# Performance work log

Hardware: AMD Instinct MI355X
Metric: run time of the kernel (lower is better)

## Reference

```python
import jax, jax.numpy as jnp
import numpy as np

H = 16  # num_attention_heads


def setup_inputs() -> dict:
    key = jax.random.key(0)
    k1, k2, k3 = jax.random.split(key, 3)
    B, S, E = 2, 2048, 1024
    return {
        "hidden_states": jax.random.normal(k1, (B, S, E), dtype=jnp.float32),
        "W_attn": jax.random.normal(k2, (E, 3 * E), dtype=jnp.float32) * 0.02,
        "b_attn": jnp.zeros((3 * E,), dtype=jnp.float32),
        "W_proj": jax.random.normal(k3, (E, E), dtype=jnp.float32) * 0.02,
        "b_proj": jnp.zeros((E,), dtype=jnp.float32),
    }


def reference(hidden_states, W_attn, b_attn, W_proj, b_proj):
    B, S, E = hidden_states.shape
    hd = E // H
    # Conv1D: x @ W + b -> [B, S, 3E]
    qkv = hidden_states @ W_attn + b_attn
    # Faithful to module: _split_heads with 3*head_dim FIRST, then split q/k/v.
    # i.e. per-head slice of size 3*hd is [q_h | k_h | v_h] (interleaved layout).
    qkv = qkv.reshape(B, S, H, 3 * hd).transpose(0, 2, 1, 3)  # [B, H, S, 3*hd]
    q, k, v = jnp.split(qkv, 3, axis=-1)                      # each [B, H, S, hd]
    # scores, scaled by sqrt(head_dim) (value.size(-1) ** 0.5)
    scores = jnp.einsum("bhqd,bhkd->bhqk", q, k) / jnp.asarray(hd, q.dtype) ** 0.5
    # causal mask via where with masked_bias = -10000.0 (not -inf), as in module
    causal = jnp.tril(jnp.ones((S, S), dtype=bool))
    scores = jnp.where(causal, scores, jnp.asarray(-10000.0, scores.dtype))
    attn_weights = jax.nn.softmax(scores, axis=-1)  # dropout p=0 -> identity
    attn_out = jnp.einsum("bhqk,bhkd->bhqd", attn_weights, v)
    attn_out = attn_out.transpose(0, 2, 1, 3).reshape(B, S, E)  # merge heads
    return attn_out @ W_proj + b_proj
```

## Files before the change

### kernel.cpp

```cpp
#include <hip/hip_runtime.h>
#include <hip/hip_bf16.h>


typedef __attribute__((ext_vector_type(4))) float f32x4;
typedef __attribute__((ext_vector_type(8))) short short8;
typedef __attribute__((ext_vector_type(2))) unsigned int uint2v;

#define AS1 __attribute__((address_space(1)))
#define AS3 __attribute__((address_space(3)))

__device__ __forceinline__ void load_lds16(const void* g, void* l) {
    __builtin_amdgcn_global_load_lds((const AS1 void*)g, (AS3 void*)l, 16, 0, 0);
}

__device__ __forceinline__ unsigned short f2bf(float f) {
    union { float f; unsigned int u; } v; v.f = f;
    unsigned int r = v.u + 0x7FFFu + ((v.u >> 16) & 1u);
    return (unsigned short)(r >> 16);
}

__device__ __forceinline__ int cvt_pk_bf16(float lo, float hi) {
    int r;
    asm("v_cvt_pk_bf16_f32 %0, %1, %2" : "=v"(r) : "v"(lo), "v"(hi));
    return r;
}

__device__ __forceinline__ void transpose_tile(
    const float* __restrict__ W, unsigned short* __restrict__ Wt,
    int K, int N, int bx, int by, int t) {
    __shared__ float tile[32][33];
    int k0 = by * 32, n0 = bx * 32;
    int r = t >> 3, c = (t & 7) * 4;
    float4 v = *(const float4*)&W[(size_t)(k0 + r) * N + n0 + c];
    tile[r][c] = v.x; tile[r][c + 1] = v.y; tile[r][c + 2] = v.z; tile[r][c + 3] = v.w;
    __syncthreads();
    int n = t >> 3; int kk = (t & 7) * 4;
    ushort4 o;
    o.x = f2bf(tile[kk + 0][n]);
    o.y = f2bf(tile[kk + 1][n]);
    o.z = f2bf(tile[kk + 2][n]);
    o.w = f2bf(tile[kk + 3][n]);
    *(ushort4*)&Wt[(size_t)(n0 + n) * K + k0 + kk] = o;
}

__global__ __launch_bounds__(256) void prep(
    const float* __restrict__ hs, unsigned short* __restrict__ Xb,
    const float* __restrict__ W_attn, unsigned short* __restrict__ WaT,
    const float* __restrict__ W_proj, unsigned short* __restrict__ WpT) {
    int bid = blockIdx.x, t = threadIdx.x;
    if (bid < 4096) {
        int i = (bid * 256 + t) * 4;
        float4 v = *(const float4*)(hs + i);
        ushort4 o;
        o.x = f2bf(v.x); o.y = f2bf(v.y); o.z = f2bf(v.z); o.w = f2bf(v.w);
        *(ushort4*)(Xb + i) = o;
    } else if (bid < 7168) {
        int r = bid - 4096;
        transpose_tile(W_attn, WaT, 1024, 3072, r % 96, r / 96, t);
    } else {
        int r = bid - 7168;
        transpose_tile(W_proj, WpT, 1024, 1024, r % 32, r / 32, t);
    }
}

__global__ __launch_bounds__(256) void gemm_qkv(
    const unsigned short* __restrict__ A,
    const unsigned short* __restrict__ Bt,
    const float* __restrict__ bias,
    unsigned short* __restrict__ qk, unsigned short* __restrict__ Vt,
    int M, int N, int K) {
    __shared__ unsigned short Sh[2][8192];
    unsigned short* Tb = &Sh[0][0];
    const int t = threadIdx.x, wave = t >> 6, lane = t & 63;
    const int l15 = lane & 15, quad = lane >> 4;
    const int m0 = blockIdx.y * 128, n0 = blockIdx.x * 128;
    const int srow = wave * 32 + (lane >> 2);
    const int sch = (lane & 3) * 8;
    const unsigned short* Ag = A + (size_t)(m0 + srow) * K + sch;
    const unsigned short* Bg = Bt + (size_t)(n0 + srow) * K + sch;
    const int wOff = wave * 1024;
    const int wm = (wave >> 1) * 64, wn = (wave & 1) * 64;
    f32x4 acc[4][4] = {};
    const int NSTEP = K / 32;
    load_lds16(Ag, &Sh[0][wOff]);
    load_lds16(Ag + (size_t)16 * K, &Sh[0][wOff + 512]);
    load_lds16(Bg, &Sh[0][4096 + wOff]);
    load_lds16(Bg + (size_t)16 * K, &Sh[0][4096 + wOff + 512]);
    for (int kt = 0; kt < NSTEP; ++kt) {
        const int cur = kt & 1;
        const unsigned short* As = &Sh[cur][0];
        const unsigned short* Bs = &Sh[cur][4096];
        __syncthreads();
        if (kt + 1 < NSTEP) {
            const int k1 = (kt + 1) * 32;
            unsigned short* An = &Sh[cur ^ 1][0];
            unsigned short* Bn = &Sh[cur ^ 1][4096];
            load_lds16(Ag + k1, An + wOff);
            load_lds16(Ag + k1 + (size_t)16 * K, An + wOff + 512);
            load_lds16(Bg + k1, Bn + wOff);
            load_lds16(Bg + k1 + (size_t)16 * K, Bn + wOff + 512);
        }
        short8 af[4], bf[4];
#pragma unroll
        for (int i = 0; i < 4; ++i) {
            af[i] = *(const short8*)&As[(wm + i * 16 + l15) * 32 + quad * 8];
            bf[i] = *(const short8*)&Bs[(wn + i * 16 + l15) * 32 + quad * 8];
        }
        __builtin_amdgcn_s_setprio(1);
#pragma unroll
        for (int mt = 0; mt < 4; ++mt)
#pragma unroll
            for (int nt = 0; nt < 4; ++nt)
                acc[mt][nt] = __builtin_amdgcn_mfma_f32_16x16x32_bf16(af[mt], bf[nt], acc[mt][nt], 0, 0, 0);
        __builtin_amdgcn_s_setprio(0);
    }
    __syncthreads();
    const int rem = n0 % 192;
#pragma unroll
    for (int mt = 0; mt < 4; ++mt) {
        int mrow = m0 + wm + mt * 16 + quad * 4;
#pragma unroll
        for (int nt = 0; nt < 4; ++nt) {
            int col = n0 + wn + nt * 16 + l15;
            float bv = bias[col];
            int h = col / 192;
            int j = col - h * 192;
            if (j < 128) {
                float sc = (j < 64) ? 0.125f : 1.0f;
#pragma unroll
                for (int r = 0; r < 4; ++r)
                    qk[(size_t)(mrow + r) * 2048 + h * 128 + j] = f2bf((acc[mt][nt][r] + bv) * sc);
            } else {
                int d = j - 128;
                int s_local = wm + mt * 16 + quad * 4;
                ushort4 pk;
                pk.x = f2bf(acc[mt][nt][0] + bv);
                pk.y = f2bf(acc[mt][nt][1] + bv);
                pk.z = f2bf(acc[mt][nt][2] + bv);
                pk.w = f2bf(acc[mt][nt][3] + bv);
                *(ushort4*)&Tb[d * 136 + s_local] = pk;
            }
        }
    }
    if (rem != 0) {
        __syncthreads();
        int vhalf = (rem == 64) ? 1 : 0;
        int h = (n0 + vhalf * 64) / 192;
        int b = m0 >> 11;
        unsigned short* vbase = Vt + ((size_t)(b * 16 + h) * 64) * 2048 + (m0 & 2047);
        int drow = t >> 4, ch = (t & 15) * 8;
#pragma unroll
        for (int rr = 0; rr < 4; ++rr) {
            int d = rr * 16 + drow;
            *(uint4*)(vbase + (size_t)d * 2048 + ch) = *(const uint4*)&Tb[d * 136 + ch];
        }
    }
}

__global__ __launch_bounds__(256) void gemm_proj(
    const unsigned short* __restrict__ A,
    const unsigned short* __restrict__ Bt,
    const float* __restrict__ bias,
    float* __restrict__ C, int M, int N, int K) {
    __shared__ unsigned short Sh[2][6144];
    const int t = threadIdx.x, wave = t >> 6, lane = t & 63;
    const int l15 = lane & 15, quad = lane >> 4;
    const int m0 = blockIdx.y * 128, n0 = blockIdx.x * 64;
    const int srowA = wave * 32 + (lane >> 2);
    const int sch = (lane & 3) * 8;
    const unsigned short* Ag = A + (size_t)(m0 + srowA) * K + sch;
    const unsigned short* Bg = Bt + (size_t)(n0 + wave * 16 + (lane >> 2)) * K + sch;
    const int aOff = wave * 1024, bOff = wave * 512;
    const int wm = (wave >> 1) * 64, wn = (wave & 1) * 32;
    f32x4 acc[4][2] = {};
    const int NSTEP = K / 32;
    load_lds16(Ag, &Sh[0][aOff]);
    load_lds16(Ag + (size_t)16 * K, &Sh[0][aOff + 512]);
    load_lds16(Bg, &Sh[0][4096 + bOff]);
    for (int kt = 0; kt < NSTEP; ++kt) {
        const int cur = kt & 1;
        const unsigned short* As = &Sh[cur][0];
        const unsigned short* Bs = &Sh[cur][4096];
        __syncthreads();
        if (kt + 1 < NSTEP) {
            const int k1 = (kt + 1) * 32;
            load_lds16(Ag + k1, &Sh[cur ^ 1][aOff]);
            load_lds16(Ag + k1 + (size_t)16 * K, &Sh[cur ^ 1][aOff + 512]);
            load_lds16(Bg + k1, &Sh[cur ^ 1][4096 + bOff]);
        }
        short8 af[4], bf[2];
#pragma unroll
        for (int i = 0; i < 4; ++i)
            af[i] = *(const short8*)&As[(wm + i * 16 + l15) * 32 + quad * 8];
#pragma unroll
        for (int i = 0; i < 2; ++i)
            bf[i] = *(const short8*)&Bs[(wn + i * 16 + l15) * 32 + quad * 8];
        __builtin_amdgcn_s_setprio(1);
#pragma unroll
        for (int mt = 0; mt < 4; ++mt)
#pragma unroll
            for (int nt = 0; nt < 2; ++nt)
                acc[mt][nt] = __builtin_amdgcn_mfma_f32_16x16x32_bf16(af[mt], bf[nt], acc[mt][nt], 0, 0, 0);
        __builtin_amdgcn_s_setprio(0);
    }
#pragma unroll
    for (int mt = 0; mt < 4; ++mt) {
        int mrow = m0 + wm + mt * 16 + quad * 4;
#pragma unroll
        for (int nt = 0; nt < 2; ++nt) {
            int col = n0 + wn + nt * 16 + l15;
            float bv = bias[col];
#pragma unroll
            for (int r = 0; r < 4; ++r)
                C[(size_t)(mrow + r) * N + col] = acc[mt][nt][r] + bv;
        }
    }
}

__device__ __forceinline__ void build_af(const int (&pk)[4][2], int qpar, short8 (&af)[2]) {
#pragma unroll
    for (int km = 0; km < 2; ++km) {
        uint2v r0 = __builtin_amdgcn_permlane32_swap(
            (unsigned)pk[2 * km][0], (unsigned)pk[2 * km + 1][0], false, false);
        uint2v r1 = __builtin_amdgcn_permlane32_swap(
            (unsigned)pk[2 * km][1], (unsigned)pk[2 * km + 1][1], false, false);
        int Ap0 = (int)r0[0], Bp0 = (int)r0[1];
        int Ap1 = (int)r1[0], Bp1 = (int)r1[1];
        int z0 = qpar ? Ap0 : Bp0;
        int z1 = qpar ? Ap1 : Bp1;
        int w0 = __builtin_amdgcn_ds_swizzle(z0, 0x401F);
        int w1 = __builtin_amdgcn_ds_swizzle(z1, 0x401F);
        int f0 = qpar ? w0 : Ap0, f1 = qpar ? w1 : Ap1;
        int g0 = qpar ? Bp0 : w0, g1 = qpar ? Bp1 : w1;
        int4 v = {f0, f1, g0, g1};
        af[km] = __builtin_bit_cast(short8, v);
    }
}

__global__ __launch_bounds__(512, 4) void attn3(
    const unsigned short* __restrict__ qk,
    const unsigned short* __restrict__ Vt,
    unsigned short* __restrict__ out) {
    const int S = 2048;
    __shared__ unsigned short Ks[2][64][72];
    __shared__ unsigned short Vts[2][64][72];
    const int t = threadIdx.x, wave = t >> 6, lane = t & 63;
    const int l15 = lane & 15, quad = lane >> 4, qpar = quad & 1;
    const int bid = blockIdx.x;
    const int qt = (bid < 256) ? (15 - (bid >> 5)) : ((bid - 256) >> 5);
    const int bh = bid & 31;
    const int b = bh >> 4, h = bh & 15;
    const unsigned short* qkb = qk + (size_t)b * S * 2048 + h * 128;
    const unsigned short* vtb = Vt + (size_t)bh * 64 * 2048;

    const int q0 = qt * 128 + wave * 16;
    short8 qf[2];
#pragma unroll
    for (int km = 0; km < 2; ++km)
        qf[km] = *(const short8*)(qkb + (size_t)(q0 + l15) * 2048 + km * 32 + quad * 8);
    f32x4 o[4] = {};
    float lrun = 0.f;

    const int srow8 = t >> 3, chunk8 = (t & 7) * 8;
    const int KT = qt * 2 + 2;

    uint4 kreg = *(const uint4*)(qkb + (size_t)srow8 * 2048 + 64 + chunk8);
    uint4 vreg = *(const uint4*)(vtb + (size_t)srow8 * 2048 + chunk8);

    const int qg = q0 + l15;
    const int qmax = q0 + 15;

    for (int kt = 0; kt < KT; ++kt) {
        const int cur = kt & 1;
        *(uint4*)&Ks[cur][srow8][chunk8] = kreg;
        *(uint4*)&Vts[cur][srow8][chunk8] = vreg;
        __syncthreads();
        if (kt + 1 < KT) {
            int kn = (kt + 1) * 64;
            kreg = *(const uint4*)(qkb + (size_t)(kn + srow8) * 2048 + 64 + chunk8);
            vreg = *(const uint4*)(vtb + (size_t)srow8 * 2048 + kn + chunk8);
        }
        const int kb = kt * 64;
        if (kb > qmax) continue;

        f32x4 s[4] = {};
        __builtin_amdgcn_s_setprio(1);
#pragma unroll
        for (int km = 0; km < 2; ++km)
#pragma unroll
            for (int nt = 0; nt < 4; ++nt) {
                short8 kf = *(const short8*)&Ks[cur][nt * 16 + l15][km * 32 + quad * 8];
                s[nt] = __builtin_amdgcn_mfma_f32_16x16x32_bf16(kf, qf[km], s[nt], 0, 0, 0);
            }
        __builtin_amdgcn_s_setprio(0);

        if (kb + 63 > q0) {
            const int ka = kb + quad * 4;
#pragma unroll
            for (int nt = 0; nt < 4; ++nt)
#pragma unroll
                for (int r = 0; r < 4; ++r)
                    if (ka + nt * 16 + r > qg) s[nt][r] = -1e30f;
        }

        int pk[4][2];
        float a0 = 0.f;
#pragma unroll
        for (int nt = 0; nt < 4; ++nt) {
            float pa[4];
#pragma unroll
            for (int r = 0; r < 4; ++r) {
                pa[r] = __expf(s[nt][r]);
                a0 += pa[r];
            }
            pk[nt][0] = cvt_pk_bf16(pa[0], pa[1]);
            pk[nt][1] = cvt_pk_bf16(pa[2], pa[3]);
        }
        lrun += a0;

        short8 af[2];
        build_af(pk, qpar, af);

        __builtin_amdgcn_s_setprio(1);
#pragma unroll
        for (int km = 0; km < 2; ++km)
#pragma unroll
            for (int nt = 0; nt < 4; ++nt) {
                short8 vf = *(const short8*)&Vts[cur][nt * 16 + l15][km * 32 + quad * 8];
                o[nt] = __builtin_amdgcn_mfma_f32_16x16x32_bf16(af[km], vf, o[nt], 0, 0, 0);
            }
        __builtin_amdgcn_s_setprio(0);
    }

    float t0 = lrun + __shfl_xor(lrun, 16);
    t0 += __shfl_xor(t0, 32);
    unsigned short* ob = out + (size_t)b * S * 1024 + h * 64;
#pragma unroll
    for (int r = 0; r < 4; ++r) {
        float i0 = 1.0f / __shfl(t0, quad * 4 + r);
        size_t r0 = (size_t)(q0 + quad * 4 + r) * 1024;
#pragma unroll
        for (int nt = 0; nt < 4; ++nt)
            ob[r0 + nt * 16 + l15] = f2bf(o[nt][r] * i0);
    }
}

extern "C" void kernel_launch(void* const* d_in, const int* in_sizes, int n_in,
                              void* d_out, int out_size, void* d_ws, size_t ws_size,
                              hipStream_t stream) {
    const float* hs     = (const float*)d_in[0];
    const float* W_attn = (const float*)d_in[1];
    const float* b_attn = (const float*)d_in[2];
    const float* W_proj = (const float*)d_in[3];
    const float* b_proj = (const float*)d_in[4];
    float* out = (float*)d_out;

    const int B = 2, S = 2048, E = 1024;
    const int M = B * S;
    const int N3 = 3 * E;

    unsigned short* Xb  = (unsigned short*)d_ws;
    unsigned short* WaT = Xb + (size_t)M * E;
    unsigned short* WpT = WaT + (size_t)N3 * E;
    unsigned short* qkb = WpT + (size_t)E * E;
    unsigned short* Vt  = qkb + (size_t)M * 2048;
    unsigned short* ao  = Vt + (size_t)M * E;

    prep<<<dim3(8192), 256, 0, stream>>>(hs, Xb, W_attn, WaT, W_proj, WpT);

    gemm_qkv<<<dim3(N3 / 128, M / 128), 256, 0, stream>>>(Xb, WaT, b_attn, qkb, Vt, M, N3, E);

    attn3<<<dim3(512), 512, 0, stream>>>(qkb, Vt, ao);

    gemm_proj<<<dim3(E / 64, M / 128), 256, 0, stream>>>(ao, WpT, b_proj, out, M, E, E);
}
```

Baseline: 176.1 us.

## Rewrite attention kernel with 32x32x16 MFMA tiles and swizzled LDS

```diff
diff --git a/kernel.cpp b/kernel.cpp
--- a/kernel.cpp
+++ b/kernel.cpp
@@ -3,6 +3,7 @@
 
 
 typedef __attribute__((ext_vector_type(4))) float f32x4;
+typedef __attribute__((ext_vector_type(16))) float f32x16;
 typedef __attribute__((ext_vector_type(8))) short short8;
 typedef __attribute__((ext_vector_type(2))) unsigned int uint2v;
 
@@ -217,35 +218,15 @@
     }
 }
 
-__device__ __forceinline__ void build_af(const int (&pk)[4][2], int qpar, short8 (&af)[2]) {
-#pragma unroll
-    for (int km = 0; km < 2; ++km) {
-        uint2v r0 = __builtin_amdgcn_permlane32_swap(
-            (unsigned)pk[2 * km][0], (unsigned)pk[2 * km + 1][0], false, false);
-        uint2v r1 = __builtin_amdgcn_permlane32_swap(
-            (unsigned)pk[2 * km][1], (unsigned)pk[2 * km + 1][1], false, false);
-        int Ap0 = (int)r0[0], Bp0 = (int)r0[1];
-        int Ap1 = (int)r1[0], Bp1 = (int)r1[1];
-        int z0 = qpar ? Ap0 : Bp0;
-        int z1 = qpar ? Ap1 : Bp1;
-        int w0 = __builtin_amdgcn_ds_swizzle(z0, 0x401F);
-        int w1 = __builtin_amdgcn_ds_swizzle(z1, 0x401F);
-        int f0 = qpar ? w0 : Ap0, f1 = qpar ? w1 : Ap1;
-        int g0 = qpar ? Bp0 : w0, g1 = qpar ? Bp1 : w1;
-        int4 v = {f0, f1, g0, g1};
-        af[km] = __builtin_bit_cast(short8, v);
-    }
-}
-
-__global__ __launch_bounds__(512, 4) void attn3(
+__global__ __launch_bounds__(256) void attn4(
     const unsigned short* __restrict__ qk,
     const unsigned short* __restrict__ Vt,
     unsigned short* __restrict__ out) {
     const int S = 2048;
-    __shared__ unsigned short Ks[2][64][72];
-    __shared__ unsigned short Vts[2][64][72];
+    __shared__ unsigned short Ks[2][4096];
+    __shared__ unsigned short Vts[2][4096];
     const int t = threadIdx.x, wave = t >> 6, lane = t & 63;
-    const int l15 = lane & 15, quad = lane >> 4, qpar = quad & 1;
+    const int l31 = lane & 31, half = lane >> 5;
     const int bid = blockIdx.x;
     const int qt = (bid < 256) ? (15 - (bid >> 5)) : ((bid - 256) >> 5);
     const int bh = bid & 31;
@@ -253,95 +234,120 @@
     const unsigned short* qkb = qk + (size_t)b * S * 2048 + h * 128;
     const unsigned short* vtb = Vt + (size_t)bh * 64 * 2048;
 
-    const int q0 = qt * 128 + wave * 16;
-    short8 qf[2];
-#pragma unroll
-    for (int km = 0; km < 2; ++km)
-        qf[km] = *(const short8*)(qkb + (size_t)(q0 + l15) * 2048 + km * 32 + quad * 8);
-    f32x4 o[4] = {};
+    const int q0 = qt * 128 + wave * 32;
+    short8 qf[4];
+#pragma unroll
+    for (int km = 0; km < 4; ++km)
+        qf[km] = *(const short8*)(qkb + (size_t)(q0 + l31) * 2048 + km * 16 + half * 8);
+
+    f32x16 o[2] = {};
     float lrun = 0.f;
 
-    const int srow8 = t >> 3, chunk8 = (t & 7) * 8;
+    const int srow = t >> 2;
+    const int c16a = (t & 3) * 2, c16b = c16a + 1;
+    const int swzA = srow * 64 + ((c16a ^ (srow & 7)) * 8);
+    const int swzB = srow * 64 + ((c16b ^ (srow & 7)) * 8);
     const int KT = qt * 2 + 2;
 
-    uint4 kreg = *(const uint4*)(qkb + (size_t)srow8 * 2048 + 64 + chunk8);
-    uint4 vreg = *(const uint4*)(vtb + (size_t)srow8 * 2048 + chunk8);
-
-    const int qg = q0 + l15;
-    const int qmax = q0 + 15;
+    uint4 kr0 = *(const uint4*)(qkb + (size_t)srow * 2048 + 64 + c16a * 8);
+    uint4 kr1 = *(const uint4*)(qkb + (size_t)srow * 2048 + 64 + c16b * 8);
+    uint4 vr0 = *(const uint4*)(vtb + (size_t)srow * 2048 + c16a * 8);
+    uint4 vr1 = *(const uint4*)(vtb + (size_t)srow * 2048 + c16b * 8);
+
+    const int qmax = q0 + 31;
+    const int ksw = l31 & 7;
+    int chs[4];
+#pragma unroll
+    for (int km = 0; km < 4; ++km)
+        chs[km] = ((km * 2 + half) ^ ksw) * 8;
+    const int krow = l31 * 64;
 
     for (int kt = 0; kt < KT; ++kt) {
         const int cur = kt & 1;
-        *(uint4*)&Ks[cur][srow8][chunk8] = kreg;
-        *(uint4*)&Vts[cur][srow8][chunk8] = vreg;
+        *(uint4*)&Ks[cur][swzA] = kr0;
+        *(uint4*)&Ks[cur][swzB] = kr1;
+        *(uint4*)&Vts[cur][swzA] = vr0;
+        *(uint4*)&Vts[cur][swzB] = vr1;
         __syncthreads();
         if (kt + 1 < KT) {
-            int kn = (kt + 1) * 64;
-            kreg = *(const uint4*)(qkb + (size_t)(kn + srow8) * 2048 + 64 + chunk8);
-            vreg = *(const uint4*)(vtb + (size_t)srow8 * 2048 + kn + chunk8);
+            const int kn = (kt + 1) * 64;
+            kr0 = *(const uint4*)(qkb + (size_t)(kn + srow) * 2048 + 64 + c16a * 8);
+            kr1 = *(const uint4*)(qkb + (size_t)(kn + srow) * 2048 + 64 + c16b * 8);
+            vr0 = *(const uint4*)(vtb + (size_t)srow * 2048 + kn + c16a * 8);
+            vr1 = *(const uint4*)(vtb + (size_t)srow * 2048 + kn + c16b * 8);
         }
         const int kb = kt * 64;
         if (kb > qmax) continue;
 
-        f32x4 s[4] = {};
+        f32x16 s[2] = {};
         __builtin_amdgcn_s_setprio(1);
 #pragma unroll
-        for (int km = 0; km < 2; ++km)
-#pragma unroll
-            for (int nt = 0; nt < 4; ++nt) {
-                short8 kf = *(const short8*)&Ks[cur][nt * 16 + l15][km * 32 + quad * 8];
-                s[nt] = __builtin_amdgcn_mfma_f32_16x16x32_bf16(kf, qf[km], s[nt], 0, 0, 0);
+        for (int nt = 0; nt < 2; ++nt)
+#pragma unroll
+            for (int km = 0; km < 4; ++km) {
+                short8 kf = *(const short8*)&Ks[cur][nt * 2048 + krow + chs[km]];
+                s[nt] = __builtin_amdgcn_mfma_f32_32x32x16_bf16(kf, qf[km], s[nt], 0, 0, 0);
             }
         __builtin_amdgcn_s_setprio(0);
 
         if (kb + 63 > q0) {
-            const int ka = kb + quad * 4;
-#pragma unroll
-            for (int nt = 0; nt < 4; ++nt)
-#pragma unroll
-                for (int r = 0; r < 4; ++r)
-                    if (ka + nt * 16 + r > qg) s[nt][r] = -1e30f;
-        }
-
-        int pk[4][2];
+#pragma unroll
+            for (int nt = 0; nt < 2; ++nt)
+#pragma unroll
+                for (int r = 0; r < 16; ++r) {
+                    int kg = kb + nt * 32 + (r & 3) + 8 * (r >> 2) + 4 * half;
+                    if (kg > q0 + l31) s[nt][r] = -1e30f;
+                }
+        }
+
+        int gd[2][4][2];
         float a0 = 0.f;
 #pragma unroll
-        for (int nt = 0; nt < 4; ++nt) {
-            float pa[4];
-#pragma unroll
-            for (int r = 0; r < 4; ++r) {
-                pa[r] = __expf(s[nt][r]);
-                a0 += pa[r];
+        for (int nt = 0; nt < 2; ++nt)
+#pragma unroll
+            for (int g = 0; g < 4; ++g) {
+                float e0 = __expf(s[nt][4 * g + 0]);
+                float e1 = __expf(s[nt][4 * g + 1]);
+                float e2 = __expf(s[nt][4 * g + 2]);
+                float e3 = __expf(s[nt][4 * g + 3]);
+                a0 += (e0 + e1) + (e2 + e3);
+                gd[nt][g][0] = cvt_pk_bf16(e0, e1);
+                gd[nt][g][1] = cvt_pk_bf16(e2, e3);
             }
-            pk[nt][0] = cvt_pk_bf16(pa[0], pa[1]);
-            pk[nt][1] = cvt_pk_bf16(pa[2], pa[3]);
-        }
         lrun += a0;
 
-        short8 af[2];
-        build_af(pk, qpar, af);
+        short8 paf[4];
+#pragma unroll
+        for (int km = 0; km < 4; ++km) {
+            const int nt = km >> 1, m = km & 1;
+            uint2v w0 = __builtin_amdgcn_permlane32_swap(
+                (unsigned)gd[nt][2 * m][0], (unsigned)gd[nt][2 * m + 1][0], false, false);
+            uint2v w1 = __builtin_amdgcn_permlane32_swap(
+                (unsigned)gd[nt][2 * m][1], (unsigned)gd[nt][2 * m + 1][1], false, false);
+            int4 v = {(int)w0[0], (int)w1[0], (int)w0[1], (int)w1[1]};
+            paf[km] = __builtin_bit_cast(short8, v);
+        }
 
         __builtin_amdgcn_s_setprio(1);
 #pragma unroll
-        for (int km = 0; km < 2; ++km)
-#pragma unroll
-            for (int nt = 0; nt < 4; ++nt) {
-                short8 vf = *(const short8*)&Vts[cur][nt * 16 + l15][km * 32 + quad * 8];
-                o[nt] = __builtin_amdgcn_mfma_f32_16x16x32_bf16(af[km], vf, o[nt], 0, 0, 0);
+        for (int nt2 = 0; nt2 < 2; ++nt2)
+#pragma unroll
+            for (int km = 0; km < 4; ++km) {
+                short8 vf = *(const short8*)&Vts[cur][nt2 * 2048 + krow + chs[km]];
+                o[nt2] = __builtin_amdgcn_mfma_f32_32x32x16_bf16(paf[km], vf, o[nt2], 0, 0, 0);
             }
         __builtin_amdgcn_s_setprio(0);
     }
 
-    float t0 = lrun + __shfl_xor(lrun, 16);
-    t0 += __shfl_xor(t0, 32);
+    float tot = lrun + __shfl_xor(lrun, 32);
     unsigned short* ob = out + (size_t)b * S * 1024 + h * 64;
 #pragma unroll
-    for (int r = 0; r < 4; ++r) {
-        float i0 = 1.0f / __shfl(t0, quad * 4 + r);
-        size_t r0 = (size_t)(q0 + quad * 4 + r) * 1024;
-#pragma unroll
-        for (int nt = 0; nt < 4; ++nt)
-            ob[r0 + nt * 16 + l15] = f2bf(o[nt][r] * i0);
+    for (int r = 0; r < 16; ++r) {
+        int ql = (r & 3) + 8 * (r >> 2) + 4 * half;
+        float inv = 1.0f / __shfl(tot, ql);
+        size_t row = (size_t)(q0 + ql) * 1024;
+        ob[row + l31] = f2bf(o[0][r] * inv);
+        ob[row + 32 + l31] = f2bf(o[1][r] * inv);
     }
 }
 
@@ -370,7 +376,7 @@
 
     gemm_qkv<<<dim3(N3 / 128, M / 128), 256, 0, stream>>>(Xb, WaT, b_attn, qkb, Vt, M, N3, E);
 
-    attn3<<<dim3(512), 512, 0, stream>>>(qkb, Vt, ao);
+    attn4<<<dim3(512), 256, 0, stream>>>(qkb, Vt, ao);
 
     gemm_proj<<<dim3(E / 64, M / 128), 256, 0, stream>>>(ao, WpT, b_proj, out, M, E, E);
 }
```

After: 175.1 us. No clear change (-0.6%).
